# Kernel optimization log

Measured on AMD Instinct MI355X. Metric: run time of the kernel, lower is better.

## Reference

```python
import jax, jax.numpy as jnp
import numpy as np


def setup_inputs() -> dict:
    key = jax.random.key(0)
    k1, k2 = jax.random.split(key)
    B, L, K, D = 131072, 4, 1024, 128
    residual = jax.random.normal(k1, (B, D), dtype=jnp.float32)
    codebooks = jax.random.normal(k2, (L, K, D), dtype=jnp.float32) * 0.1
    return {"residual": residual, "codebooks": codebooks}


def reference(residual, codebooks):
    """Residual VQ: per level, nearest-codeword assignment, gather, subtract.

    residual:  [B, D]
    codebooks: [L, K, D]
    Returns (quantized [B, D], codes [B, L] int32).
    """

    def step(res, emb):
        # squared L2 distances: ||r||^2 + ||e||^2 - 2 r.e  -> [B, K]
        x2 = jnp.sum(res * res, axis=1, keepdims=True)
        e2 = jnp.sum(emb * emb, axis=1)
        scores = x2 + e2 - 2.0 * (res @ emb.T)
        idx = jnp.argmin(scores, axis=1)            # [B]
        q = emb[idx]                                # gather [B, D]
        return res - q, (q, idx)

    _, (qs, idxs) = jax.lax.scan(step, residual, codebooks)
    quantized = jnp.sum(qs, axis=0)                 # [B, D]
    codes = idxs.T                                  # [B, L]
    return quantized, codes
```

## Files before the change

### kernel.cpp

```cpp
#include <hip/hip_runtime.h>
#include <math.h>


#define D_DIM 128
#define K_CB  1024
#define L_LVL 4
#define LK    (L_LVL * K_CB)
#define LKD   (LK * D_DIM)
#define NT2   16
#define TILE_ELEMS 8192
#define MARGIN_P5 6e-4f

typedef __bf16 bf16x8 __attribute__((ext_vector_type(8)));
typedef float  f32x16 __attribute__((ext_vector_type(16)));

static __device__ __forceinline__ float mulr(float a, float b) {
    float p = a * b; asm volatile("" : "+v"(p)); return p;
}

__global__ void rvq_prep(const float* __restrict__ cb,
                         __bf16* __restrict__ hi, __bf16* __restrict__ lo,
                         float* __restrict__ e2p, unsigned* __restrict__ flagcnt) {
    int j = blockIdx.x * blockDim.x + threadIdx.x;
    if (j == 0) *flagcnt = 0;
    const int lane = j & 63, kk = (j >> 6) & 7, s = (j >> 9) & 1,
              t = (j >> 10) & 15, lv = j >> 14;
    const int row  = lv * K_CB + t * 64 + s * 32 + (lane & 31);
    const int elem = kk * 16 + (lane >> 5) * 8;
    const float* src = cb + (size_t)row * D_DIM + elem;
    float4 a = *(const float4*)src;
    float4 b = *(const float4*)(src + 4);
    float f[8] = {a.x, a.y, a.z, a.w, b.x, b.y, b.z, b.w};
    bf16x8 hv, lvv;
    #pragma unroll
    for (int e = 0; e < 8; ++e) {
        __bf16 h = (__bf16)f[e];
        hv[e]  = h;
        lvv[e] = (__bf16)(f[e] - (float)h);
    }
    *(bf16x8*)(hi + (size_t)j * 8) = hv;
    *(bf16x8*)(lo + (size_t)j * 8) = lvv;

    if (j < LK) {
        const float* ep = cb + (size_t)j * D_DIM;
        float r8[8];
        #pragma unroll
        for (int q = 0; q < 8; ++q) r8[q] = mulr(ep[q], ep[q]);
        #pragma unroll
        for (int bb = 1; bb < 16; ++bb)
            #pragma unroll
            for (int q = 0; q < 8; ++q) r8[q] += mulr(ep[bb * 8 + q], ep[bb * 8 + q]);
        e2p[j] = ((r8[0] + r8[1]) + (r8[2] + r8[3])) + ((r8[4] + r8[5]) + (r8[6] + r8[7]));
    }
}

static __device__ __forceinline__ void stage_tile(
    const __bf16* srcTile, __bf16* dst, int wave, int lane) {
    #pragma unroll
    for (int c = 0; c < 4; ++c) {
        const int it = wave * 4 + c;
        __builtin_amdgcn_global_load_lds(
            (const __attribute__((address_space(1))) void*)(srcTile + it * 512 + lane * 8),
            (__attribute__((address_space(3))) void*)(dst + it * 512), 16, 0, 0);
    }
}

#define MFMA(A, Bv, C) __builtin_amdgcn_mfma_f32_32x32x16_bf16(A, Bv, C, 0, 0, 0)

static __device__ __forceinline__ float pack5(float sc, unsigned pk5) {
    unsigned u = __float_as_uint(sc);
    return __uint_as_float(((u + 16u) & ~31u) | pk5);
}

__global__ __launch_bounds__(256)
void rvq_mfma(const float* __restrict__ residual,
              const float* __restrict__ codebooks,
              const __bf16* __restrict__ cbh, const __bf16* __restrict__ cbl,
              const float* __restrict__ e2p,
              unsigned* __restrict__ flagcnt, unsigned* __restrict__ flaglist,
              unsigned flagcap, float* __restrict__ out, int B) {
    __shared__ __align__(16) __bf16 bufh[2][TILE_ELEMS];
    __shared__ float e2s[K_CB];
    __shared__ int   bidxs[L_LVL][128];
    __shared__ unsigned char flg[128];

    const int tid  = threadIdx.x;
    const int wave = tid >> 6;
    const int lane = tid & 63;
    const int col  = lane & 31;
    const int h    = lane >> 5;
    const int rb   = wave * 32;
    const int grow = blockIdx.x * 128 + rb + col;

    if (tid < 128) flg[tid] = 0;

    bf16x8 Ah[8], Al[8];
    {
        const float* rowp = residual + (size_t)grow * D_DIM;
        #pragma unroll
        for (int kk = 0; kk < 8; ++kk) {
            const int d0 = kk * 16 + h * 8;
            float4 a = *(const float4*)(rowp + d0);
            float4 b = *(const float4*)(rowp + d0 + 4);
            float f[8] = {a.x, a.y, a.z, a.w, b.x, b.y, b.z, b.w};
            #pragma unroll
            for (int e = 0; e < 8; ++e) {
                __bf16 hh = (__bf16)f[e];
                Ah[kk][e] = hh;
                Al[kk][e] = (__bf16)(f[e] - (float)hh);
            }
        }
    }

    for (int l = 0; l < L_LVL; ++l) {
        const __bf16* cbhL = cbh + (size_t)l * NT2 * TILE_ELEMS;
        const __bf16* cblL = cbl + (size_t)l * NT2 * TILE_ELEMS;

        ((float4*)e2s)[tid] = ((const float4*)(e2p + l * K_CB))[tid];
        asm volatile("s_waitcnt vmcnt(0)" ::: "memory");

        float rbest[16], rbest2[16];
        #pragma unroll
        for (int s = 0; s < 16; ++s) { rbest[s] = 0.f; rbest2[s] = 0.f; }

        stage_tile(cbhL + 0 * TILE_ELEMS, &bufh[0][0], wave, lane);
        stage_tile(cbhL + 1 * TILE_ELEMS, &bufh[1][0], wave, lane);

        for (int t = 0; t < NT2; ++t) {
            const int cur = t & 1;
            const __bf16* bh  = &bufh[cur][0];
            const __bf16* blT = cblL + (size_t)t * TILE_ELEMS;

            if (t == 0) asm volatile("s_waitcnt vmcnt(4) lgkmcnt(0)" ::: "memory");
            __builtin_amdgcn_s_barrier();
            __builtin_amdgcn_sched_barrier(0);

            bf16x8 Blr[8];
            #pragma unroll
            for (int kk = 0; kk < 8; ++kk)
                Blr[kk] = *(const bf16x8*)(blT + kk * 512 + lane * 8);

            const float e2i0 = fmaf(-0.5f, e2s[t * 64 + col], 16.f);
            const float e2i1 = fmaf(-0.5f, e2s[t * 64 + 32 + col], 16.f);
            f32x16 acc0, acc1;
            #pragma unroll
            for (int s = 0; s < 16; ++s) { acc0[s] = e2i0; acc1[s] = e2i1; }

            __builtin_amdgcn_s_setprio(1);
            #pragma unroll
            for (int kk = 0; kk < 8; ++kk) {
                bf16x8 Bh0 = *(const bf16x8*)(bh + kk * 512 + lane * 8);
                bf16x8 Bh1 = *(const bf16x8*)(bh + 4096 + kk * 512 + lane * 8);
                acc0 = MFMA(Ah[kk], Bh0, acc0);
                acc0 = MFMA(Al[kk], Bh0, acc0);
                acc1 = MFMA(Ah[kk], Bh1, acc1);
                acc1 = MFMA(Al[kk], Bh1, acc1);
            }
            asm volatile("s_waitcnt vmcnt(0)" ::: "memory");
            __builtin_amdgcn_sched_barrier(0);
            #pragma unroll
            for (int kk = 0; kk < 8; ++kk) acc0 = MFMA(Ah[kk], Blr[kk], acc0);
            __builtin_amdgcn_s_setprio(0);

            #pragma unroll
            for (int kk = 0; kk < 8; ++kk)
                Blr[kk] = *(const bf16x8*)(blT + 4096 + kk * 512 + lane * 8);

            __builtin_amdgcn_sched_barrier(0);
            __builtin_amdgcn_s_barrier();
            asm volatile("" ::: "memory");
            if (t + 2 < NT2)
                stage_tile(cbhL + (size_t)(t + 2) * TILE_ELEMS, &bufh[cur][0], wave, lane);

            const unsigned pk0 = 31u - (unsigned)(t * 2);
            #pragma unroll
            for (int s = 0; s < 16; ++s) {
                float p0 = pack5(acc0[s], pk0);
                rbest2[s] = __builtin_amdgcn_fmed3f(p0, rbest[s], rbest2[s]);
                rbest[s]  = fmaxf(rbest[s], p0);
            }

            if (t + 2 < NT2) asm volatile("s_waitcnt vmcnt(4)" ::: "memory");
            else             asm volatile("s_waitcnt vmcnt(0)" ::: "memory");
            __builtin_amdgcn_sched_barrier(0);
            __builtin_amdgcn_s_setprio(1);
            #pragma unroll
            for (int kk = 0; kk < 8; ++kk) acc1 = MFMA(Ah[kk], Blr[kk], acc1);
            __builtin_amdgcn_s_setprio(0);

            const unsigned pk1 = 31u - (unsigned)(t * 2 + 1);
            #pragma unroll
            for (int s = 0; s < 16; ++s) {
                float p1 = pack5(acc1[s], pk1);
                rbest2[s] = __builtin_amdgcn_fmed3f(p1, rbest[s], rbest2[s]);
                rbest[s]  = fmaxf(rbest[s], p1);
            }
        }

        #pragma unroll
        for (int s = 0; s < 16; ++s) {
            float b = rbest[s], b2 = rbest2[s];
            int   c = col;
            #pragma unroll
            for (int m = 1; m <= 16; m <<= 1) {
                float bo  = __shfl_xor(b,  m, 64);
                float b2o = __shfl_xor(b2, m, 64);
                int   co  = __shfl_xor(c,  m, 64);
                float nb2 = fmaxf(fminf(b, bo), fmaxf(b2, b2o));
                if (bo > b || (bo == b && co < c)) { b = bo; c = co; }
                b2 = nb2;
            }
            const int rloc = (s & 3) + 8 * (s >> 2) + 4 * h;
            if (col == 0) {
                int idx5 = 31 - (int)(__float_as_uint(b) & 31u);
                bidxs[l][rb + rloc] = idx5 * 32 + c;
                if (b - b2 <= MARGIN_P5) flg[rb + rloc] = 1;
            }
        }
        __syncthreads();

        {
            const int bi = bidxs[l][rb + col];
            const float* qp = codebooks + ((size_t)l * K_CB + bi) * D_DIM;
            #pragma unroll
            for (int kk = 0; kk < 8; ++kk) {
                const int d0 = kk * 16 + h * 8;
                float4 qa = *(const float4*)(qp + d0);
                float4 qb = *(const float4*)(qp + d0 + 4);
                float q[8] = {qa.x, qa.y, qa.z, qa.w, qb.x, qb.y, qb.z, qb.w};
                #pragma unroll
                for (int e = 0; e < 8; ++e) {
                    float r = ((float)Ah[kk][e] + (float)Al[kk][e]) - q[e];
                    __bf16 hh = (__bf16)r;
                    Ah[kk][e] = hh;
                    Al[kk][e] = (__bf16)(r - (float)hh);
                }
            }
        }
    }

    {
        const float* rowp = residual + (size_t)grow * D_DIM;
        float* op = out + (size_t)grow * D_DIM;
        #pragma unroll
        for (int kk = 0; kk < 8; ++kk) {
            const int d0 = kk * 16 + h * 8;
            float4 a = *(const float4*)(rowp + d0);
            float4 b = *(const float4*)(rowp + d0 + 4);
            float f[8] = {a.x, a.y, a.z, a.w, b.x, b.y, b.z, b.w};
            float o[8];
            #pragma unroll
            for (int e = 0; e < 8; ++e)
                o[e] = f[e] - ((float)Ah[kk][e] + (float)Al[kk][e]);
            *(float4*)(op + d0)     = make_float4(o[0], o[1], o[2], o[3]);
            *(float4*)(op + d0 + 4) = make_float4(o[4], o[5], o[6], o[7]);
        }
    }
    if (tid < 128) {
        int row = blockIdx.x * 128 + tid;
        float4* cp = (float4*)(out + (size_t)B * D_DIM + (size_t)row * L_LVL);
        *cp = make_float4((float)bidxs[0][tid], (float)bidxs[1][tid],
                          (float)bidxs[2][tid], (float)bidxs[3][tid]);
        if (flg[tid]) {
            unsigned pos = atomicAdd(flagcnt, 1u);
            if (pos < flagcap) flaglist[pos] = row;
        }
    }
}

__global__ __launch_bounds__(256, 1)
void rvq_fixup(const float* __restrict__ residual,
               const float* __restrict__ codebooks,
               const float* __restrict__ e2p,
               const unsigned* __restrict__ flagcnt,
               const unsigned* __restrict__ flaglist,
               unsigned flagcap, float* __restrict__ out, int B) {
    __shared__ float rbuf[D_DIM];
    __shared__ float r0buf[D_DIM];
    __shared__ float x2s;
    __shared__ float redS[256];
    __shared__ int   redK[256];
    __shared__ int   codes_s[L_LVL];

    unsigned n = *flagcnt;
    if (n > flagcap) n = flagcap;

    for (unsigned b = blockIdx.x; b < n; b += gridDim.x) {
        int row = (int)flaglist[b];
        if (threadIdx.x < 32) {
            float4 v = ((const float4*)(residual + (size_t)row * D_DIM))[threadIdx.x];
            *(float4*)&rbuf[threadIdx.x * 4]  = v;
            *(float4*)&r0buf[threadIdx.x * 4] = v;
        }
        __syncthreads();

        for (int l = 0; l < L_LVL; ++l) {
            const float* cbl = codebooks + (size_t)l * K_CB * D_DIM;
            if (threadIdx.x == 0) {
                float r8[8];
                #pragma unroll
                for (int q = 0; q < 8; ++q) r8[q] = mulr(rbuf[q], rbuf[q]);
                for (int bb = 1; bb < 16; ++bb)
                    #pragma unroll
                    for (int q = 0; q < 8; ++q) r8[q] += mulr(rbuf[bb * 8 + q], rbuf[bb * 8 + q]);
                x2s = ((r8[0] + r8[1]) + (r8[2] + r8[3])) + ((r8[4] + r8[5]) + (r8[6] + r8[7]));
            }
            __syncthreads();
            float x2 = x2s;

            float bS = 3.4e38f;
            int   bK = 0x7fffffff;
            for (int m = 0; m < 4; ++m) {
                int k = threadIdx.x + m * 256;
                const float4* ek = (const float4*)(cbl + (size_t)k * D_DIM);
                double dd = 0.0;
                for (int c = 0; c < 32; ++c) {
                    float4 v = ek[c];
                    dd = fma((double)v.x, (double)rbuf[c * 4 + 0], dd);
                    dd = fma((double)v.y, (double)rbuf[c * 4 + 1], dd);
                    dd = fma((double)v.z, (double)rbuf[c * 4 + 2], dd);
                    dd = fma((double)v.w, (double)rbuf[c * 4 + 3], dd);
                }
                float M = (float)dd;
                float A = x2 + e2p[l * K_CB + k];
                float S = A - 2.0f * M;
                if (S < bS || (S == bS && k < bK)) { bS = S; bK = k; }
            }
            redS[threadIdx.x] = bS; redK[threadIdx.x] = bK;
            __syncthreads();
            for (int s = 128; s > 0; s >>= 1) {
                if (threadIdx.x < (unsigned)s) {
                    float So = redS[threadIdx.x + s];
                    int   Ko = redK[threadIdx.x + s];
                    if (So < redS[threadIdx.x] ||
                        (So == redS[threadIdx.x] && Ko < redK[threadIdx.x])) {
                        redS[threadIdx.x] = So; redK[threadIdx.x] = Ko;
                    }
                }
                __syncthreads();
            }
            int bi = redK[0];
            if (threadIdx.x == 0) codes_s[l] = bi;
            if (threadIdx.x < 32) {
                float4 q = ((const float4*)(cbl + (size_t)bi * D_DIM))[threadIdx.x];
                float4* p = (float4*)&rbuf[threadIdx.x * 4];
                float4 x = *p;
                x.x -= q.x; x.y -= q.y; x.z -= q.z; x.w -= q.w;
                *p = x;
            }
            __syncthreads();
        }

        if (threadIdx.x < 32) {
            float4 a = *(float4*)&r0buf[threadIdx.x * 4];
            float4 r = *(float4*)&rbuf[threadIdx.x * 4];
            ((float4*)(out + (size_t)row * D_DIM))[threadIdx.x] =
                make_float4(a.x - r.x, a.y - r.y, a.z - r.z, a.w - r.w);
        }
        if (threadIdx.x == 0) {
            float4* cp = (float4*)(out + (size_t)B * D_DIM + (size_t)row * L_LVL);
            *cp = make_float4((float)codes_s[0], (float)codes_s[1],
                              (float)codes_s[2], (float)codes_s[3]);
        }
        __syncthreads();
    }
}

extern "C" void kernel_launch(void* const* d_in, const int* in_sizes, int n_in,
                              void* d_out, int out_size, void* d_ws, size_t ws_size,
                              hipStream_t stream) {
    const float* residual  = (const float*)d_in[0];
    const float* codebooks = (const float*)d_in[1];
    float* out = (float*)d_out;
    int B = in_sizes[0] / D_DIM;

    const size_t E2_BYTES = LK * sizeof(float);
    const size_t CB_BYTES = (size_t)LKD * 2;

    float*    e2p      = (float*)d_ws;
    __bf16*   cbh      = (__bf16*)((char*)d_ws + E2_BYTES);
    __bf16*   cblo     = (__bf16*)((char*)d_ws + E2_BYTES + CB_BYTES);
    unsigned* flagcnt  = (unsigned*)((char*)d_ws + E2_BYTES + 2 * CB_BYTES);
    unsigned* flaglist = flagcnt + 16;
    unsigned  flagcap  = (unsigned)((ws_size - (E2_BYTES + 2 * CB_BYTES + 64)) / 4);
    if (flagcap > (unsigned)B) flagcap = (unsigned)B;

    hipLaunchKernelGGL(rvq_prep, dim3(LKD / 8 / 256), dim3(256), 0, stream,
                       codebooks, cbh, cblo, e2p, flagcnt);
    hipLaunchKernelGGL(rvq_mfma, dim3(B / 128), dim3(256), 0, stream,
                       residual, codebooks, cbh, cblo, e2p,
                       flagcnt, flaglist, flagcap, out, B);
    hipLaunchKernelGGL(rvq_fixup, dim3(512), dim3(256), 0, stream,
                       residual, codebooks, e2p, flagcnt, flaglist, flagcap, out, B);
}
```

Measured before the change: 782.4 us.

## Tighten fixup margin, add occupancy hint, split fixup dot accumulators, double fixup grid

```diff
diff --git a/kernel.cpp b/kernel.cpp
--- a/kernel.cpp
+++ b/kernel.cpp
@@ -9,7 +9,7 @@
 #define LKD   (LK * D_DIM)
 #define NT2   16
 #define TILE_ELEMS 8192
-#define MARGIN_P5 6e-4f
+#define MARGIN_P5 4.5e-4f
 
 typedef __bf16 bf16x8 __attribute__((ext_vector_type(8)));
 typedef float  f32x16 __attribute__((ext_vector_type(16)));
@@ -72,7 +72,7 @@
     return __uint_as_float(((u + 16u) & ~31u) | pk5);
 }
 
-__global__ __launch_bounds__(256)
+__global__ __launch_bounds__(256, 3)
 void rvq_mfma(const float* __restrict__ residual,
               const float* __restrict__ codebooks,
               const __bf16* __restrict__ cbh, const __bf16* __restrict__ cbl,
@@ -313,15 +313,27 @@
             for (int m = 0; m < 4; ++m) {
                 int k = threadIdx.x + m * 256;
                 const float4* ek = (const float4*)(cbl + (size_t)k * D_DIM);
-                double dd = 0.0;
-                for (int c = 0; c < 32; ++c) {
-                    float4 v = ek[c];
-                    dd = fma((double)v.x, (double)rbuf[c * 4 + 0], dd);
-                    dd = fma((double)v.y, (double)rbuf[c * 4 + 1], dd);
-                    dd = fma((double)v.z, (double)rbuf[c * 4 + 2], dd);
-                    dd = fma((double)v.w, (double)rbuf[c * 4 + 3], dd);
+                double dd0 = 0.0, dd1 = 0.0, dd2 = 0.0, dd3 = 0.0;
+                for (int c = 0; c < 32; c += 4) {
+                    float4 v0 = ek[c], v1 = ek[c + 1], v2 = ek[c + 2], v3 = ek[c + 3];
+                    dd0 = fma((double)v0.x, (double)rbuf[c * 4 + 0], dd0);
+                    dd0 = fma((double)v0.y, (double)rbuf[c * 4 + 1], dd0);
+                    dd0 = fma((double)v0.z, (double)rbuf[c * 4 + 2], dd0);
+                    dd0 = fma((double)v0.w, (double)rbuf[c * 4 + 3], dd0);
+                    dd1 = fma((double)v1.x, (double)rbuf[c * 4 + 4], dd1);
+                    dd1 = fma((double)v1.y, (double)rbuf[c * 4 + 5], dd1);
+                    dd1 = fma((double)v1.z, (double)rbuf[c * 4 + 6], dd1);
+                    dd1 = fma((double)v1.w, (double)rbuf[c * 4 + 7], dd1);
+                    dd2 = fma((double)v2.x, (double)rbuf[c * 4 + 8], dd2);
+                    dd2 = fma((double)v2.y, (double)rbuf[c * 4 + 9], dd2);
+                    dd2 = fma((double)v2.z, (double)rbuf[c * 4 + 10], dd2);
+                    dd2 = fma((double)v2.w, (double)rbuf[c * 4 + 11], dd2);
+                    dd3 = fma((double)v3.x, (double)rbuf[c * 4 + 12], dd3);
+                    dd3 = fma((double)v3.y, (double)rbuf[c * 4 + 13], dd3);
+                    dd3 = fma((double)v3.z, (double)rbuf[c * 4 + 14], dd3);
+                    dd3 = fma((double)v3.w, (double)rbuf[c * 4 + 15], dd3);
                 }
-                float M = (float)dd;
+                float M = (float)((dd0 + dd1) + (dd2 + dd3));
                 float A = x2 + e2p[l * K_CB + k];
                 float S = A - 2.0f * M;
                 if (S < bS || (S == bS && k < bK)) { bS = S; bK = k; }
@@ -390,6 +402,6 @@
     hipLaunchKernelGGL(rvq_mfma, dim3(B / 128), dim3(256), 0, stream,
                        residual, codebooks, cbh, cblo, e2p,
                        flagcnt, flaglist, flagcap, out, B);
-    hipLaunchKernelGGL(rvq_fixup, dim3(512), dim3(256), 0, stream,
+    hipLaunchKernelGGL(rvq_fixup, dim3(1024), dim3(256), 0, stream,
                        residual, codebooks, e2p, flagcnt, flaglist, flagcap, out, B);
 }
```

New measurement: 764.6 us. 1.02x faster.
